# Performance work log

Hardware: AMD Instinct MI355X
Metric: run time of the kernel (lower is better)

## Reference

```python
import jax, jax.numpy as jnp
import numpy as np

EPS = 1e-5  # LayerNorm eps (torch default)
K_NN = 16   # matches init kwarg k


def _knn_idx(pos, k):
    # pos: (B,N,3) -> (B,N,k) indices of k nearest points (sorted by distance,
    # includes self at slot 0), matching pytorch3d knn_points(return_sorted=True).
    sq = jnp.sum(pos * pos, axis=-1)                                   # (B,N)
    d2 = sq[:, :, None] + sq[:, None, :] - 2.0 * jnp.einsum('bnd,bmd->bnm', pos, pos)
    _, idx = jax.lax.top_k(-d2, k)                                     # ascending distance
    return idx


def _gather(feats, idx):
    # feats: (B,N,C), idx: (B,N,K) -> (B,N,K,C)
    return jax.vmap(lambda f, i: f[i])(feats, idx)


def _ln(x, g, b):
    mu = jnp.mean(x, axis=-1, keepdims=True)
    var = jnp.mean((x - mu) ** 2, axis=-1, keepdims=True)
    return (x - mu) * jax.lax.rsqrt(var + EPS) * g + b


def setup_inputs() -> dict:
    key = jax.random.key(0)
    B, N, D, H = 2, 4096, 128, 12
    ks = jax.random.split(key, 16)
    s = 0.05
    f32 = jnp.float32
    return {
        'x': jax.random.normal(ks[0], (B, N, D), f32),
        'pos': jax.random.normal(ks[1], (B, N, 3), f32),
        # linear projections (bias=False)
        'w_q': jax.random.normal(ks[2], (D, D), f32) * s,
        'w_k': jax.random.normal(ks[3], (D, D), f32) * s,
        'w_v': jax.random.normal(ks[4], (D, D), f32) * s,
        # pos_mlp: Linear(3,H) -> LN(H) -> ReLU -> Linear(H,D)
        'pos_w1': jax.random.normal(ks[5], (H, 3), f32) * s,
        'pos_b1': jnp.zeros((H,), f32),
        'pos_g': jnp.ones((H,), f32),
        'pos_beta': jnp.zeros((H,), f32),
        'pos_w2': jax.random.normal(ks[6], (D, H), f32) * s,
        'pos_b2': jnp.zeros((D,), f32),
        # attn_mlp: Linear(D,D) -> LN(D) -> ReLU -> Linear(D,D)
        'attn_w1': jax.random.normal(ks[7], (D, D), f32) * s,
        'attn_b1': jnp.zeros((D,), f32),
        'attn_g': jnp.ones((D,), f32),
        'attn_beta': jnp.zeros((D,), f32),
        'attn_w2': jax.random.normal(ks[8], (D, D), f32) * s,
        'attn_b2': jnp.zeros((D,), f32),
    }


def reference(x, pos, w_q, w_k, w_v,
              pos_w1, pos_b1, pos_g, pos_beta, pos_w2, pos_b2,
              attn_w1, attn_b1, attn_g, attn_beta, attn_w2, attn_b2):
    idx = _knn_idx(pos, K_NN)                        # (B,N,K)
    q = x @ w_q.T                                    # (B,N,D)
    kf = _gather(x @ w_k.T, idx)                     # (B,N,K,D)
    vf = _gather(x @ w_v.T, idx)                     # (B,N,K,D)
    pos_rel = pos[:, :, None, :] - _gather(pos, idx)  # (B,N,K,3)
    # pos_mlp
    pe = _ln(pos_rel @ pos_w1.T + pos_b1, pos_g, pos_beta)
    pe = jax.nn.relu(pe) @ pos_w2.T + pos_b2         # (B,N,K,D)
    # attn_mlp on (q - k + pos_enc)
    w = q[:, :, None, :] - kf + pe
    w = _ln(w @ attn_w1.T + attn_b1, attn_g, attn_beta)
    w = jax.nn.relu(w) @ attn_w2.T + attn_b2         # (B,N,K,D)
    attn = jax.nn.softmax(w, axis=2)                 # softmax over neighbor dim
    return jnp.einsum('bnkd,bnkd->bnd', attn, vf + pe)
```

## Files before the change

### kernel.cpp

```cpp
#include <hip/hip_runtime.h>
#include <hip/hip_bf16.h>
#include <math.h>

#define BATCH 2
#define NPTS 4096
#define DIM 128
#define HID 12
#define KNN 16
#define NSLOT 24
#define BCAP 192
#define BCT 64

#define FOLD_BLOCKS 128
#define M1_BLOCKS 32
#define PRE_BLOCKS (FOLD_BLOCKS + M1_BLOCKS + 4)
#define KNN_BLOCKS (BATCH * NPTS / 4)

typedef __attribute__((ext_vector_type(8))) short short8;
typedef __attribute__((ext_vector_type(4))) float f32x4;

__device__ __forceinline__ short f2b(float f) {
  unsigned u = __float_as_uint(f);
  unsigned r = (u + 0x7fffu + ((u >> 16) & 1u)) >> 16;
  return (short)r;
}
__device__ __forceinline__ float b2f(short h) {
  return __uint_as_float(((unsigned)(unsigned short)h) << 16);
}

#define BITONIC64(v, vi)                                                     \
  {                                                                          \
    _Pragma("unroll") for (int k_ = 2; k_ <= 64; k_ <<= 1) {                 \
      _Pragma("unroll") for (int j_ = k_ >> 1; j_ >= 1; j_ >>= 1) {          \
        const float ov_ = __shfl_xor((v), j_);                               \
        const int oi_ = __shfl_xor((vi), j_);                                \
        const bool up_ = ((lane & k_) == 0);                                 \
        const bool lowpos_ = ((lane & j_) == 0);                             \
        const bool keep_min_ = (lowpos_ == up_);                             \
        const bool lt_ = (ov_ < (v)) || (ov_ == (v) && oi_ < (vi));          \
        const bool take_ = keep_min_ ? lt_ : !lt_;                           \
        if (take_) { (v) = ov_; (vi) = oi_; }                                \
      }                                                                      \
    }                                                                        \
  }

__device__ void knn_body(int bid, const float* __restrict__ pos,
                         int* __restrict__ knn_out) {
  __shared__ float bd_s[4][BCAP];
  __shared__ int bi_s[4][BCAP];

  const int t = threadIdx.x;
  const int w = t >> 6;
  const int lane = t & 63;
  const int n = (bid << 2) + w;
  const int b = n >> 12;
  const int qn = n & (NPTS - 1);

  float* bdl = &bd_s[w][0];
  int* bil = &bi_s[w][0];

  const float* pb = pos + b * NPTS * 3;
  const float qx = pb[qn * 3 + 0];
  const float qy = pb[qn * 3 + 1];
  const float qz = pb[qn * 3 + 2];

  const bool is_slot = (lane < NSLOT);
  float vald, thr;
  int validx;
  int bcount = 0;

  {
    const float2* pp = (const float2*)(pb + lane * 6);
    const float2 u0 = pp[0], u1 = pp[1], u2 = pp[2];
    float dx = qx - u0.x, dy = qy - u0.y, dz = qz - u1.x;
    float v = fmaf(dx, dx, fmaf(dy, dy, dz * dz));
    int vi = lane * 2;
    dx = qx - u1.y; dy = qy - u2.x; dz = qz - u2.y;
    const float d2b = fmaf(dx, dx, fmaf(dy, dy, dz * dz));

    BITONIC64(v, vi)
    vald = is_slot ? v : __builtin_inff();
    validx = is_slot ? vi : 0x7fffffff;
    const float v15 = __shfl(v, 15);
    thr = v15 + v15 * 1e-5f;

    const unsigned long long m = __ballot(d2b < thr);
    if (m) {
      const unsigned lt = __builtin_amdgcn_mbcnt_hi(
          (unsigned)(m >> 32), __builtin_amdgcn_mbcnt_lo((unsigned)m, 0u));
      if (d2b < thr) { bdl[lt] = d2b; bil[lt] = 2 * lane + 1; }
      bcount = (int)__builtin_popcountll(m);
    }
  }

  const float2* pp = (const float2*)(pb + 384 + lane * 6);
  float2 A0 = pp[0], A1 = pp[1], A2 = pp[2];
  pp = (const float2*)(pb + 768 + lane * 6);
  float2 B0 = pp[0], B1 = pp[1], B2 = pp[2];

#pragma unroll 1
  for (int it = 1; it < NPTS / 128; ++it) {
    const float2 c0 = A0, c1v = A1, c2 = A2;
    A0 = B0; A1 = B1; A2 = B2;
    if (it + 2 < NPTS / 128) {
      pp = (const float2*)(pb + (it + 2) * 384 + lane * 6);
      B0 = pp[0]; B1 = pp[1]; B2 = pp[2];
    }
    float dx = qx - c0.x, dy = qy - c0.y, dz = qz - c1v.x;
    const float e2a = fmaf(dx, dx, fmaf(dy, dy, dz * dz));
    dx = qx - c1v.y; dy = qy - c2.x; dz = qz - c2.y;
    const float e2b = fmaf(dx, dx, fmaf(dy, dy, dz * dz));

    if (bcount >= BCT) {
#pragma unroll 1
      while (bcount > 0) {
        const int take = bcount < 40 ? bcount : 40;
        float mv = __builtin_inff();
        int mi = 0x7fffffff;
        if (lane < NSLOT) { mv = vald; mi = validx; }
        else if (lane - NSLOT < take) {
          mv = bdl[bcount - take + lane - NSLOT];
          mi = bil[bcount - take + lane - NSLOT];
        }
        BITONIC64(mv, mi)
        if (is_slot) { vald = mv; validx = mi; }
        bcount -= take;
      }
      const float v15 = __shfl(vald, 15);
      thr = v15 + v15 * 1e-5f;
    }

    {
      const unsigned long long m = __ballot(e2a < thr);
      if (m) {
        const unsigned lt = __builtin_amdgcn_mbcnt_hi(
            (unsigned)(m >> 32), __builtin_amdgcn_mbcnt_lo((unsigned)m, 0u));
        if (e2a < thr) { bdl[bcount + lt] = e2a; bil[bcount + lt] = it * 128 + 2 * lane; }
        bcount += (int)__builtin_popcountll(m);
      }
    }
    {
      const unsigned long long m = __ballot(e2b < thr);
      if (m) {
        const unsigned lt = __builtin_amdgcn_mbcnt_hi(
            (unsigned)(m >> 32), __builtin_amdgcn_mbcnt_lo((unsigned)m, 0u));
        if (e2b < thr) { bdl[bcount + lt] = e2b; bil[bcount + lt] = it * 128 + 2 * lane + 1; }
        bcount += (int)__builtin_popcountll(m);
      }
    }
  }

#pragma unroll 1
  while (bcount > 0) {
    const int take = bcount < 40 ? bcount : 40;
    float mv = __builtin_inff();
    int mi = 0x7fffffff;
    if (lane < NSLOT) { mv = vald; mi = validx; }
    else if (lane - NSLOT < take) {
      mv = bdl[bcount - take + lane - NSLOT];
      mi = bil[bcount - take + lane - NSLOT];
    }
    BITONIC64(mv, mi)
    if (is_slot) { vald = mv; validx = mi; }
    bcount -= take;
  }

  double d2e = 1e300;
  if (is_slot) {
    const double ex = (double)qx - (double)pb[validx * 3 + 0];
    const double ey = (double)qy - (double)pb[validx * 3 + 1];
    const double ez = (double)qz - (double)pb[validx * 3 + 2];
    d2e = ex * ex + ey * ey + ez * ez;
  }
  int rank = 0;
#pragma unroll 1
  for (int j = 0; j < NSLOT; ++j) {
    const double dj = __shfl(d2e, j);
    const int ij = __shfl(validx, j);
    if (dj < d2e || (dj == d2e && ij < validx)) ++rank;
  }
  if (is_slot && rank < KNN) knn_out[((b << 12) + qn) * KNN + rank] = validx;
}

__device__ void fold_body(int bid, const float* __restrict__ aw1,
                          const float* __restrict__ wq, const float* __restrict__ wk,
                          short* __restrict__ WqaHi, short* __restrict__ WqaLo,
                          short* __restrict__ WkaHi, short* __restrict__ WkaLo) {
  const float* w = (bid < 64) ? wq : wk;
  short* oh = (bid < 64) ? WqaHi : WkaHi;
  short* ol = (bid < 64) ? WqaLo : WkaLo;
  const int row = ((bid & 63) << 1) + (threadIdx.x >> 7);
  const int i = threadIdx.x & 127;
  float acc = 0.f;
  for (int j = 0; j < 128; ++j) acc = fmaf(aw1[row * 128 + j], w[j * 128 + i], acc);
  const short h = f2b(acc);
  oh[row * 128 + i] = h;
  ol[row * 128 + i] = f2b(acc - b2f(h));
}

__device__ void m1_body(int bid, const float* __restrict__ aw1,
                        const float* __restrict__ pw2, const float* __restrict__ pb2,
                        const float* __restrict__ ab1,
                        short* __restrict__ M1b, float* __restrict__ c1) {
  const int t = threadIdx.x;
  const int wid = t >> 6, lane = t & 63;
  const int o = bid * 4 + wid;
  const float a0 = aw1[o * 128 + lane];
  const float a1 = aw1[o * 128 + 64 + lane];

  float s = fmaf(a0, pb2[lane], a1 * pb2[64 + lane]);
#pragma unroll
  for (int off = 1; off < 64; off <<= 1) s += __shfl_xor(s, off);
  if (lane == 0) c1[o] = ab1[o] + s;

#pragma unroll
  for (int k = 0; k < HID; ++k) {
    float p = fmaf(a0, pw2[lane * HID + k], a1 * pw2[(64 + lane) * HID + k]);
#pragma unroll
    for (int off = 1; off < 64; off <<= 1) p += __shfl_xor(p, off);
    if (lane == 0) M1b[o * 32 + k] = f2b(p);
  }
  if (lane >= HID && lane < 32) M1b[o * 32 + lane] = 0;
}

__device__ void pw2b_body(const float* __restrict__ pw2, short* __restrict__ pw2b) {
  const int t = threadIdx.x;
  for (int i = t; i < 128 * 32; i += 256) {
    const int o = i >> 5, k = i & 31;
    pw2b[i] = (k < HID) ? f2b(pw2[o * HID + k]) : (short)0;
  }
}
__device__ void aw2b_body(int half, const float* __restrict__ aw2,
                          short* __restrict__ aw2b) {
  const int base = half * 8192;
  for (int i = threadIdx.x; i < 8192; i += 256) aw2b[base + i] = f2b(aw2[base + i]);
}
__device__ void wv_body(const float* __restrict__ wv, short* __restrict__ WvHi,
                        short* __restrict__ WvLo) {
  for (int i = threadIdx.x; i < 128 * 128; i += 256) {
    const float v = wv[i];
    const short h = f2b(v);
    WvHi[i] = h;
    WvLo[i] = f2b(v - b2f(h));
  }
}

__global__ __launch_bounds__(256) void knn_prep_kernel(
    const float* __restrict__ pos, int* __restrict__ knn_out,
    const float* __restrict__ aw1, const float* __restrict__ wq,
    const float* __restrict__ wk,
    short* __restrict__ WqaHi, short* __restrict__ WqaLo,
    short* __restrict__ WkaHi, short* __restrict__ WkaLo,
    const float* __restrict__ pw2, const float* __restrict__ pb2,
    const float* __restrict__ ab1, const float* __restrict__ aw2,
    const float* __restrict__ wv,
    short* __restrict__ M1b, short* __restrict__ pw2b, short* __restrict__ aw2b,
    float* __restrict__ c1, short* __restrict__ WvHi, short* __restrict__ WvLo) {
  const int bid = blockIdx.x;
  if (bid < FOLD_BLOCKS) {
    fold_body(bid, aw1, wq, wk, WqaHi, WqaLo, WkaHi, WkaLo);
  } else if (bid < FOLD_BLOCKS + M1_BLOCKS) {
    m1_body(bid - FOLD_BLOCKS, aw1, pw2, pb2, ab1, M1b, c1);
  } else if (bid == FOLD_BLOCKS + M1_BLOCKS) {
    pw2b_body(pw2, pw2b);
  } else if (bid <= FOLD_BLOCKS + M1_BLOCKS + 2) {
    aw2b_body(bid - (FOLD_BLOCKS + M1_BLOCKS + 1), aw2, aw2b);
  } else if (bid == FOLD_BLOCKS + M1_BLOCKS + 3) {
    wv_body(wv, WvHi, WvLo);
  } else {
    knn_body(bid - PRE_BLOCKS, pos, knn_out);
  }
}

__global__ __launch_bounds__(256) void proj_mfma_kernel(
    const float* __restrict__ x,
    const short* __restrict__ WqaHi, const short* __restrict__ WqaLo,
    const short* __restrict__ WkaHi, const short* __restrict__ WkaLo,
    const short* __restrict__ WvHi, const short* __restrict__ WvLo,
    short* __restrict__ QAb, short* __restrict__ KAb, short* __restrict__ Vpb) {
  const int t = threadIdx.x;
  const int wid = t >> 6, lane = t & 63;
  const int r16 = lane & 15, g4 = lane >> 4;
  const int rowbase = blockIdx.x * 32 + (wid >> 1) * 16;
  const int ch = wid & 1;

  short8 ahi[4], alo[4];
#pragma unroll
  for (int ks = 0; ks < 4; ++ks) {
    const float* xp = x + (rowbase + r16) * DIM + ks * 32 + g4 * 8;
#pragma unroll
    for (int e = 0; e < 8; ++e) {
      const float v = xp[e];
      const short h = f2b(v);
      ahi[ks][e] = h;
      alo[ks][e] = f2b(v - b2f(h));
    }
  }

  const f32x4 zero4 = {0.f, 0.f, 0.f, 0.f};
  const short* WH[3] = {WqaHi, WkaHi, WvHi};
  const short* WL[3] = {WqaLo, WkaLo, WvLo};
  short* OUT[3] = {QAb, KAb, Vpb};
#pragma unroll
  for (int mi = 0; mi < 3; ++mi) {
    const short* wh = WH[mi];
    const short* wl = WL[mi];
    short* o = OUT[mi];
#pragma unroll
    for (int q = 0; q < 4; ++q) {
      const int col = (ch * 4 + q) * 16 + r16;
      f32x4 a = zero4;
#pragma unroll
      for (int ks = 0; ks < 4; ++ks) {
        const short8 bh = *(const short8*)(wh + col * DIM + ks * 32 + g4 * 8);
        const short8 bl = *(const short8*)(wl + col * DIM + ks * 32 + g4 * 8);
        a = __builtin_amdgcn_mfma_f32_16x16x32_bf16(ahi[ks], bh, a, 0, 0, 0);
        a = __builtin_amdgcn_mfma_f32_16x16x32_bf16(alo[ks], bh, a, 0, 0, 0);
        a = __builtin_amdgcn_mfma_f32_16x16x32_bf16(ahi[ks], bl, a, 0, 0, 0);
      }
#pragma unroll
      for (int reg = 0; reg < 4; ++reg)
        o[(rowbase + g4 * 4 + reg) * DIM + (ch * 4 + q) * 16 + r16] = f2b(a[reg]);
    }
  }
}

__global__ __launch_bounds__(256) void pt_wave_kernel(
    const float* __restrict__ pos, const int* __restrict__ knn_in,
    const short* __restrict__ QAb, const short* __restrict__ KAb,
    const short* __restrict__ Vpb,
    const float* __restrict__ pw1, const float* __restrict__ pb1,
    const float* __restrict__ pg, const float* __restrict__ pbeta,
    const float* __restrict__ pb2,
    const float* __restrict__ ag, const float* __restrict__ abeta,
    const float* __restrict__ ab2, const float* __restrict__ c1,
    const short* __restrict__ M1b, const short* __restrict__ pw2b,
    const short* __restrict__ aw2b,
    float* __restrict__ out) {
  __shared__ __align__(16) short z_s[2048];
  __shared__ float red_s[2][4][16];
  __shared__ short hr_s[16][HID];

  const int t = threadIdx.x;
  const int wid = t >> 6;
  const int lane = t & 63;
  const int r16 = lane & 15;
  const int g4 = lane >> 4;
  const int n = blockIdx.x;
  const int b = n >> 12;

  int myidx = 0;
  if (lane < KNN) myidx = knn_in[n * KNN + lane];
  int jC[4];
#pragma unroll
  for (int reg = 0; reg < 4; ++reg) jC[reg] = __shfl(myidx, g4 * 4 + reg);

  const bool pm = (wid == 0) && (lane < 16);

  float rx = 0.f, ry = 0.f, rz = 0.f;
  if (pm) {
    const int jg = b * NPTS + myidx;
    rx = pos[n * 3 + 0] - pos[jg * 3 + 0];
    ry = pos[n * 3 + 1] - pos[jg * 3 + 1];
    rz = pos[n * 3 + 2] - pos[jg * 3 + 2];
  }

  float qa_[2], kav[2][4], vv[2][4];
#pragma unroll
  for (int q = 0; q < 2; ++q) {
    const int o = (wid * 2 + q) * 16 + r16;
    qa_[q] = b2f(QAb[n * DIM + o]);
#pragma unroll
    for (int reg = 0; reg < 4; ++reg) {
      const int row = b * NPTS + jC[reg];
      kav[q][reg] = b2f(KAb[row * DIM + o]);
      vv[q][reg] = b2f(Vpb[row * DIM + o]);
    }
  }

  if (pm) {
    float hr[HID];
    float mu = 0.f;
#pragma unroll
    for (int hh = 0; hh < HID; ++hh) {
      const float v = pb1[hh] + rx * pw1[hh * 3 + 0] + ry * pw1[hh * 3 + 1] +
                      rz * pw1[hh * 3 + 2];
      hr[hh] = v;
      mu += v;
    }
    mu *= (1.f / HID);
    float var = 0.f;
#pragma unroll
    for (int hh = 0; hh < HID; ++hh) { const float d = hr[hh] - mu; var = fmaf(d, d, var); }
    const float rsn = rsqrtf(var * (1.f / HID) + 1e-5f);
#pragma unroll
    for (int hh = 0; hh < HID; ++hh)
      hr_s[lane][hh] = f2b(fmaxf(fmaf((hr[hh] - mu) * rsn, pg[hh], pbeta[hh]), 0.f));
  }
  __syncthreads();

  short8 a1 = {0, 0, 0, 0, 0, 0, 0, 0};
  if (g4 == 0) {
#pragma unroll
    for (int e = 0; e < 8; ++e) a1[e] = hr_s[r16][e];
  } else if (g4 == 1) {
#pragma unroll
    for (int e = 0; e < 4; ++e) a1[e] = hr_s[r16][8 + e];
  }

  const f32x4 zero4 = {0.f, 0.f, 0.f, 0.f};
  f32x4 accw[2], accp[2];
#pragma unroll
  for (int q = 0; q < 2; ++q) {
    const int boff = ((wid * 2 + q) * 16 + r16) * 32 + g4 * 8;
    const short8 bm = *(const short8*)(M1b + boff);
    const short8 bp = *(const short8*)(pw2b + boff);
    accw[q] = __builtin_amdgcn_mfma_f32_16x16x32_bf16(a1, bm, zero4, 0, 0, 0);
    accp[q] = __builtin_amdgcn_mfma_f32_16x16x32_bf16(a1, bp, zero4, 0, 0, 0);
  }

  float w1v[2][4];
#pragma unroll
  for (int q = 0; q < 2; ++q) {
    const int o = (wid * 2 + q) * 16 + r16;
    const float base = qa_[q] + c1[o];
#pragma unroll
    for (int reg = 0; reg < 4; ++reg)
      w1v[q][reg] = accw[q][reg] + base - kav[q][reg];
  }

  {
    float ps[4], pq2[4];
#pragma unroll
    for (int reg = 0; reg < 4; ++reg) {
      ps[reg] = w1v[0][reg] + w1v[1][reg];
      pq2[reg] = fmaf(w1v[0][reg], w1v[0][reg], w1v[1][reg] * w1v[1][reg]);
    }
#pragma unroll
    for (int reg = 0; reg < 4; ++reg) {
#pragma unroll
      for (int off = 1; off <= 8; off <<= 1) {
        ps[reg] += __shfl_xor(ps[reg], off);
        pq2[reg] += __shfl_xor(pq2[reg], off);
      }
    }
    if (r16 == 0) {
#pragma unroll
      for (int reg = 0; reg < 4; ++reg) {
        red_s[0][wid][g4 * 4 + reg] = ps[reg];
        red_s[1][wid][g4 * 4 + reg] = pq2[reg];
      }
    }
  }
  __syncthreads();
  float mu[4], rs[4];
#pragma unroll
  for (int reg = 0; reg < 4; ++reg) {
    const int rr = g4 * 4 + reg;
    const float s = red_s[0][0][rr] + red_s[0][1][rr] + red_s[0][2][rr] + red_s[0][3][rr];
    const float q2 = red_s[1][0][rr] + red_s[1][1][rr] + red_s[1][2][rr] + red_s[1][3][rr];
    mu[reg] = s * (1.f / 128.f);
    const float var = q2 * (1.f / 128.f) - mu[reg] * mu[reg];
    rs[reg] = rsqrtf(var + 1e-5f);
  }

  {
    char* zb = (char*)z_s;
#pragma unroll
    for (int q = 0; q < 2; ++q) {
      const int o = (wid * 2 + q) * 16 + r16;
      const float gam = ag[o], bet = abeta[o];
#pragma unroll
      for (int reg = 0; reg < 4; ++reg) {
        const int rr = g4 * 4 + reg;
        const float zv = fmaxf(fmaf((w1v[q][reg] - mu[reg]) * rs[reg], gam, bet), 0.f);
        unsigned byte = (unsigned)(rr * 256 + o * 2);
        byte ^= ((unsigned)(rr & 7) << 4) ^ ((unsigned)(rr & 8) << 2);
        *(short*)(zb + byte) = f2b(zv);
      }
    }
  }
  __syncthreads();

  short8 a2[4];
  {
    const char* zb = (const char*)z_s;
#pragma unroll
    for (int ks = 0; ks < 4; ++ks) {
      unsigned byte = (unsigned)(r16 * 256 + ks * 64 + g4 * 16);
      byte ^= ((unsigned)(r16 & 7) << 4) ^ ((unsigned)(r16 & 8) << 2);
      a2[ks] = *(const short8*)(zb + byte);
    }
  }

  f32x4 acc2[2] = {zero4, zero4};
#pragma unroll
  for (int q = 0; q < 2; ++q) {
#pragma unroll
    for (int ks = 0; ks < 4; ++ks) {
      const short8 bw =
          *(const short8*)(aw2b + ((wid * 2 + q) * 16 + r16) * DIM + ks * 32 + g4 * 8);
      acc2[q] = __builtin_amdgcn_mfma_f32_16x16x32_bf16(a2[ks], bw, acc2[q], 0, 0, 0);
    }
  }

  float ew[2][4], inv[2];
#pragma unroll
  for (int q = 0; q < 2; ++q) {
    const float bb = ab2[(wid * 2 + q) * 16 + r16];
#pragma unroll
    for (int reg = 0; reg < 4; ++reg) ew[q][reg] = acc2[q][reg] + bb;
    float m = fmaxf(fmaxf(ew[q][0], ew[q][1]), fmaxf(ew[q][2], ew[q][3]));
    m = fmaxf(m, __shfl_xor(m, 16));
    m = fmaxf(m, __shfl_xor(m, 32));
    float s = 0.f;
#pragma unroll
    for (int reg = 0; reg < 4; ++reg) { ew[q][reg] = __expf(ew[q][reg] - m); s += ew[q][reg]; }
    s += __shfl_xor(s, 16);
    s += __shfl_xor(s, 32);
    inv[q] = 1.f / s;
  }

  float o_acc[2];
#pragma unroll
  for (int q = 0; q < 2; ++q) {
    const int o = (wid * 2 + q) * 16 + r16;
    const float pb = pb2[o];
    float acc = 0.f;
#pragma unroll
    for (int reg = 0; reg < 4; ++reg)
      acc = fmaf(ew[q][reg] * inv[q], vv[q][reg] + accp[q][reg] + pb, acc);
    acc += __shfl_xor(acc, 16);
    acc += __shfl_xor(acc, 32);
    o_acc[q] = acc;
  }
  if (g4 < 2) out[n * DIM + (wid * 2 + g4) * 16 + r16] = o_acc[g4];
}

extern "C" void kernel_launch(void* const* d_in, const int* in_sizes, int n_in,
                              void* d_out, int out_size, void* d_ws, size_t ws_size,
                              hipStream_t stream) {
  const float* x   = (const float*)d_in[0];
  const float* pos = (const float*)d_in[1];
  const float* wq  = (const float*)d_in[2];
  const float* wk  = (const float*)d_in[3];
  const float* wv  = (const float*)d_in[4];
  const float* pw1 = (const float*)d_in[5];
  const float* pb1 = (const float*)d_in[6];
  const float* pg  = (const float*)d_in[7];
  const float* pbt = (const float*)d_in[8];
  const float* pw2 = (const float*)d_in[9];
  const float* pb2 = (const float*)d_in[10];
  const float* aw1 = (const float*)d_in[11];
  const float* ab1 = (const float*)d_in[12];
  const float* ag  = (const float*)d_in[13];
  const float* abt = (const float*)d_in[14];
  const float* aw2 = (const float*)d_in[15];
  const float* ab2 = (const float*)d_in[16];
  float* out = (float*)d_out;

  char* ws = (char*)d_ws;
  int*   knn   = (int*)ws;
  short* WqaHi = (short*)(ws + 512u * 1024u);
  short* WqaLo = (short*)(ws + 544u * 1024u);
  short* WkaHi = (short*)(ws + 576u * 1024u);
  short* WkaLo = (short*)(ws + 608u * 1024u);
  short* M1b   = (short*)(ws + 640u * 1024u);
  short* pw2b  = (short*)(ws + 648u * 1024u);
  short* aw2b  = (short*)(ws + 656u * 1024u);
  float* c1    = (float*)(ws + 688u * 1024u);
  short* WvHi  = (short*)(ws + 704u * 1024u);
  short* WvLo  = (short*)(ws + 736u * 1024u);
  short* QAb   = (short*)(ws + (1u << 20));
  short* KAb   = (short*)(ws + 4u * (1u << 20));
  short* Vpb   = (short*)(ws + 7u * (1u << 20));

  knn_prep_kernel<<<PRE_BLOCKS + KNN_BLOCKS, 256, 0, stream>>>(
      pos, knn, aw1, wq, wk, WqaHi, WqaLo, WkaHi, WkaLo, pw2, pb2, ab1, aw2, wv,
      M1b, pw2b, aw2b, c1, WvHi, WvLo);
  proj_mfma_kernel<<<BATCH * NPTS / 32, 256, 0, stream>>>(
      x, WqaHi, WqaLo, WkaHi, WkaLo, WvHi, WvLo, QAb, KAb, Vpb);
  pt_wave_kernel<<<BATCH * NPTS, 256, 0, stream>>>(
      pos, knn, QAb, KAb, Vpb, pw1, pb1, pg, pbt, pb2, ag, abt, ab2, c1,
      M1b, pw2b, aw2b, out);
}
```

Before: 122.1 us.

## Split KNN scan across two waves per query and batch queries per attention block

The KNN search now gives each query point two wavefronts. Each scans half of the candidate points, and the two sorted 24-slot candidate lists are merged through shared memory with one extra bitonic sort before the exact-distance ranking. This halves the serial scan length per wave and doubles the number of KNN blocks. Separately, the attention kernel now loops over 4 query points per block, which cuts launch and block-scheduling overhead but also reduces the number of blocks. The merge adds a block barrier and an extra sort, and the batching adds a serial dependency between query points.

After: 142.0 us. 1.16x slower.

```diff
diff --git a/kernel.cpp b/kernel.cpp
--- a/kernel.cpp
+++ b/kernel.cpp
@@ -10,11 +10,12 @@
 #define NSLOT 24
 #define BCAP 192
 #define BCT 64
+#define PTQ 4
 
 #define FOLD_BLOCKS 128
 #define M1_BLOCKS 32
 #define PRE_BLOCKS (FOLD_BLOCKS + M1_BLOCKS + 4)
-#define KNN_BLOCKS (BATCH * NPTS / 4)
+#define KNN_BLOCKS (BATCH * NPTS / 2)
 
 typedef __attribute__((ext_vector_type(8))) short short8;
 typedef __attribute__((ext_vector_type(4))) float f32x4;
@@ -44,6 +45,17 @@
     }                                                                        \
   }
 
+#define KNN_EVENTS(d2v, base, odd)                                        \
+  {                                                                       \
+    unsigned long long m_ = __ballot((d2v) < thr);                        \
+    if (m_) {                                                             \
+      const unsigned lt_ = __builtin_amdgcn_mbcnt_hi(                     \
+          (unsigned)(m_ >> 32), __builtin_amdgcn_mbcnt_lo((unsigned)m_, 0u)); \
+      if ((d2v) < thr) { bdl[bcount + lt_] = (d2v); bil[bcount + lt_] = (base) + 2 * lane + (odd); } \
+      bcount += (int)__builtin_popcountll(m_);                            \
+    }                                                                     \
+  }
+
 __device__ void knn_body(int bid, const float* __restrict__ pos,
                          int* __restrict__ knn_out) {
   __shared__ float bd_s[4][BCAP];
@@ -52,9 +64,11 @@
   const int t = threadIdx.x;
   const int w = t >> 6;
   const int lane = t & 63;
-  const int n = (bid << 2) + w;
+  const int n = bid * 2 + (w >> 1);
+  const int half = w & 1;
   const int b = n >> 12;
   const int qn = n & (NPTS - 1);
+  const int base0 = half * (NPTS / 2);
 
   float* bdl = &bd_s[w][0];
   int* bil = &bi_s[w][0];
@@ -70,11 +84,11 @@
   int bcount = 0;
 
   {
-    const float2* pp = (const float2*)(pb + lane * 6);
+    const float2* pp = (const float2*)(pb + base0 * 3 + lane * 6);
     const float2 u0 = pp[0], u1 = pp[1], u2 = pp[2];
     float dx = qx - u0.x, dy = qy - u0.y, dz = qz - u1.x;
     float v = fmaf(dx, dx, fmaf(dy, dy, dz * dz));
-    int vi = lane * 2;
+    int vi = base0 + lane * 2;
     dx = qx - u1.y; dy = qy - u2.x; dz = qz - u2.y;
     const float d2b = fmaf(dx, dx, fmaf(dy, dy, dz * dz));
 
@@ -84,26 +98,20 @@
     const float v15 = __shfl(v, 15);
     thr = v15 + v15 * 1e-5f;
 
-    const unsigned long long m = __ballot(d2b < thr);
-    if (m) {
-      const unsigned lt = __builtin_amdgcn_mbcnt_hi(
-          (unsigned)(m >> 32), __builtin_amdgcn_mbcnt_lo((unsigned)m, 0u));
-      if (d2b < thr) { bdl[lt] = d2b; bil[lt] = 2 * lane + 1; }
-      bcount = (int)__builtin_popcountll(m);
-    }
-  }
-
-  const float2* pp = (const float2*)(pb + 384 + lane * 6);
+    KNN_EVENTS(d2b, base0, 1)
+  }
+
+  const float2* pp = (const float2*)(pb + (base0 + 128) * 3 + lane * 6);
   float2 A0 = pp[0], A1 = pp[1], A2 = pp[2];
-  pp = (const float2*)(pb + 768 + lane * 6);
+  pp = (const float2*)(pb + (base0 + 256) * 3 + lane * 6);
   float2 B0 = pp[0], B1 = pp[1], B2 = pp[2];
 
 #pragma unroll 1
-  for (int it = 1; it < NPTS / 128; ++it) {
+  for (int it = 1; it < NPTS / 256; ++it) {
     const float2 c0 = A0, c1v = A1, c2 = A2;
     A0 = B0; A1 = B1; A2 = B2;
-    if (it + 2 < NPTS / 128) {
-      pp = (const float2*)(pb + (it + 2) * 384 + lane * 6);
+    if (it + 2 < NPTS / 256) {
+      pp = (const float2*)(pb + (base0 + (it + 2) * 128) * 3 + lane * 6);
       B0 = pp[0]; B1 = pp[1]; B2 = pp[2];
     }
     float dx = qx - c0.x, dy = qy - c0.y, dz = qz - c1v.x;
@@ -130,24 +138,8 @@
       thr = v15 + v15 * 1e-5f;
     }
 
-    {
-      const unsigned long long m = __ballot(e2a < thr);
-      if (m) {
-        const unsigned lt = __builtin_amdgcn_mbcnt_hi(
-            (unsigned)(m >> 32), __builtin_amdgcn_mbcnt_lo((unsigned)m, 0u));
-        if (e2a < thr) { bdl[bcount + lt] = e2a; bil[bcount + lt] = it * 128 + 2 * lane; }
-        bcount += (int)__builtin_popcountll(m);
-      }
-    }
-    {
-      const unsigned long long m = __ballot(e2b < thr);
-      if (m) {
-        const unsigned lt = __builtin_amdgcn_mbcnt_hi(
-            (unsigned)(m >> 32), __builtin_amdgcn_mbcnt_lo((unsigned)m, 0u));
-        if (e2b < thr) { bdl[bcount + lt] = e2b; bil[bcount + lt] = it * 128 + 2 * lane + 1; }
-        bcount += (int)__builtin_popcountll(m);
-      }
-    }
+    KNN_EVENTS(e2a, base0 + it * 128, 0)
+    KNN_EVENTS(e2b, base0 + it * 128, 1)
   }
 
 #pragma unroll 1
@@ -165,21 +157,34 @@
     bcount -= take;
   }
 
+  if (half == 1 && lane < NSLOT) { bdl[lane] = vald; bil[lane] = validx; }
+  __syncthreads();
+  if (half == 1) return;
+
+  float mv = __builtin_inff();
+  int mi = 0x7fffffff;
+  if (lane < NSLOT) { mv = vald; mi = validx; }
+  else if (lane < 2 * NSLOT) {
+    mv = bd_s[w + 1][lane - NSLOT];
+    mi = bi_s[w + 1][lane - NSLOT];
+  }
+  BITONIC64(mv, mi)
+
   double d2e = 1e300;
   if (is_slot) {
-    const double ex = (double)qx - (double)pb[validx * 3 + 0];
-    const double ey = (double)qy - (double)pb[validx * 3 + 1];
-    const double ez = (double)qz - (double)pb[validx * 3 + 2];
+    const double ex = (double)qx - (double)pb[mi * 3 + 0];
+    const double ey = (double)qy - (double)pb[mi * 3 + 1];
+    const double ez = (double)qz - (double)pb[mi * 3 + 2];
     d2e = ex * ex + ey * ey + ez * ez;
   }
   int rank = 0;
 #pragma unroll 1
   for (int j = 0; j < NSLOT; ++j) {
     const double dj = __shfl(d2e, j);
-    const int ij = __shfl(validx, j);
-    if (dj < d2e || (dj == d2e && ij < validx)) ++rank;
-  }
-  if (is_slot && rank < KNN) knn_out[((b << 12) + qn) * KNN + rank] = validx;
+    const int ij = __shfl(mi, j);
+    if (dj < d2e || (dj == d2e && ij < mi)) ++rank;
+  }
+  if (is_slot && rank < KNN) knn_out[((b << 12) + qn) * KNN + rank] = mi;
 }
 
 __device__ void fold_body(int bid, const float* __restrict__ aw1,
@@ -346,195 +351,199 @@
   const int lane = t & 63;
   const int r16 = lane & 15;
   const int g4 = lane >> 4;
-  const int n = blockIdx.x;
-  const int b = n >> 12;
-
-  int myidx = 0;
-  if (lane < KNN) myidx = knn_in[n * KNN + lane];
-  int jC[4];
-#pragma unroll
-  for (int reg = 0; reg < 4; ++reg) jC[reg] = __shfl(myidx, g4 * 4 + reg);
-
-  const bool pm = (wid == 0) && (lane < 16);
-
-  float rx = 0.f, ry = 0.f, rz = 0.f;
-  if (pm) {
-    const int jg = b * NPTS + myidx;
-    rx = pos[n * 3 + 0] - pos[jg * 3 + 0];
-    ry = pos[n * 3 + 1] - pos[jg * 3 + 1];
-    rz = pos[n * 3 + 2] - pos[jg * 3 + 2];
-  }
-
-  float qa_[2], kav[2][4], vv[2][4];
-#pragma unroll
-  for (int q = 0; q < 2; ++q) {
-    const int o = (wid * 2 + q) * 16 + r16;
-    qa_[q] = b2f(QAb[n * DIM + o]);
-#pragma unroll
-    for (int reg = 0; reg < 4; ++reg) {
-      const int row = b * NPTS + jC[reg];
-      kav[q][reg] = b2f(KAb[row * DIM + o]);
-      vv[q][reg] = b2f(Vpb[row * DIM + o]);
-    }
-  }
-
-  if (pm) {
-    float hr[HID];
-    float mu = 0.f;
-#pragma unroll
-    for (int hh = 0; hh < HID; ++hh) {
-      const float v = pb1[hh] + rx * pw1[hh * 3 + 0] + ry * pw1[hh * 3 + 1] +
-                      rz * pw1[hh * 3 + 2];
-      hr[hh] = v;
-      mu += v;
-    }
-    mu *= (1.f / HID);
-    float var = 0.f;
-#pragma unroll
-    for (int hh = 0; hh < HID; ++hh) { const float d = hr[hh] - mu; var = fmaf(d, d, var); }
-    const float rsn = rsqrtf(var * (1.f / HID) + 1e-5f);
-#pragma unroll
-    for (int hh = 0; hh < HID; ++hh)
-      hr_s[lane][hh] = f2b(fmaxf(fmaf((hr[hh] - mu) * rsn, pg[hh], pbeta[hh]), 0.f));
-  }
-  __syncthreads();
-
-  short8 a1 = {0, 0, 0, 0, 0, 0, 0, 0};
-  if (g4 == 0) {
-#pragma unroll
-    for (int e = 0; e < 8; ++e) a1[e] = hr_s[r16][e];
-  } else if (g4 == 1) {
-#pragma unroll
-    for (int e = 0; e < 4; ++e) a1[e] = hr_s[r16][8 + e];
-  }
-
   const f32x4 zero4 = {0.f, 0.f, 0.f, 0.f};
-  f32x4 accw[2], accp[2];
-#pragma unroll
-  for (int q = 0; q < 2; ++q) {
-    const int boff = ((wid * 2 + q) * 16 + r16) * 32 + g4 * 8;
-    const short8 bm = *(const short8*)(M1b + boff);
-    const short8 bp = *(const short8*)(pw2b + boff);
-    accw[q] = __builtin_amdgcn_mfma_f32_16x16x32_bf16(a1, bm, zero4, 0, 0, 0);
-    accp[q] = __builtin_amdgcn_mfma_f32_16x16x32_bf16(a1, bp, zero4, 0, 0, 0);
-  }
-
-  float w1v[2][4];
-#pragma unroll
-  for (int q = 0; q < 2; ++q) {
-    const int o = (wid * 2 + q) * 16 + r16;
-    const float base = qa_[q] + c1[o];
-#pragma unroll
-    for (int reg = 0; reg < 4; ++reg)
-      w1v[q][reg] = accw[q][reg] + base - kav[q][reg];
-  }
-
-  {
-    float ps[4], pq2[4];
-#pragma unroll
-    for (int reg = 0; reg < 4; ++reg) {
-      ps[reg] = w1v[0][reg] + w1v[1][reg];
-      pq2[reg] = fmaf(w1v[0][reg], w1v[0][reg], w1v[1][reg] * w1v[1][reg]);
-    }
-#pragma unroll
-    for (int reg = 0; reg < 4; ++reg) {
-#pragma unroll
-      for (int off = 1; off <= 8; off <<= 1) {
-        ps[reg] += __shfl_xor(ps[reg], off);
-        pq2[reg] += __shfl_xor(pq2[reg], off);
-      }
-    }
-    if (r16 == 0) {
-#pragma unroll
-      for (int reg = 0; reg < 4; ++reg) {
-        red_s[0][wid][g4 * 4 + reg] = ps[reg];
-        red_s[1][wid][g4 * 4 + reg] = pq2[reg];
-      }
-    }
-  }
-  __syncthreads();
-  float mu[4], rs[4];
-#pragma unroll
-  for (int reg = 0; reg < 4; ++reg) {
-    const int rr = g4 * 4 + reg;
-    const float s = red_s[0][0][rr] + red_s[0][1][rr] + red_s[0][2][rr] + red_s[0][3][rr];
-    const float q2 = red_s[1][0][rr] + red_s[1][1][rr] + red_s[1][2][rr] + red_s[1][3][rr];
-    mu[reg] = s * (1.f / 128.f);
-    const float var = q2 * (1.f / 128.f) - mu[reg] * mu[reg];
-    rs[reg] = rsqrtf(var + 1e-5f);
-  }
-
-  {
-    char* zb = (char*)z_s;
+
+#pragma unroll 1
+  for (int qi = 0; qi < PTQ; ++qi) {
+    const int n = blockIdx.x * PTQ + qi;
+    const int b = n >> 12;
+
+    int myidx = 0;
+    if (lane < KNN) myidx = knn_in[n * KNN + lane];
+    int jC[4];
+#pragma unroll
+    for (int reg = 0; reg < 4; ++reg) jC[reg] = __shfl(myidx, g4 * 4 + reg);
+
+    const bool pm = (wid == 0) && (lane < 16);
+
+    float rx = 0.f, ry = 0.f, rz = 0.f;
+    if (pm) {
+      const int jg = b * NPTS + myidx;
+      rx = pos[n * 3 + 0] - pos[jg * 3 + 0];
+      ry = pos[n * 3 + 1] - pos[jg * 3 + 1];
+      rz = pos[n * 3 + 2] - pos[jg * 3 + 2];
+    }
+
+    float qa_[2], kav[2][4], vv[2][4];
 #pragma unroll
     for (int q = 0; q < 2; ++q) {
       const int o = (wid * 2 + q) * 16 + r16;
-      const float gam = ag[o], bet = abeta[o];
+      qa_[q] = b2f(QAb[n * DIM + o]);
 #pragma unroll
       for (int reg = 0; reg < 4; ++reg) {
-        const int rr = g4 * 4 + reg;
-        const float zv = fmaxf(fmaf((w1v[q][reg] - mu[reg]) * rs[reg], gam, bet), 0.f);
-        unsigned byte = (unsigned)(rr * 256 + o * 2);
-        byte ^= ((unsigned)(rr & 7) << 4) ^ ((unsigned)(rr & 8) << 2);
-        *(short*)(zb + byte) = f2b(zv);
-      }
-    }
-  }
-  __syncthreads();
-
-  short8 a2[4];
-  {
-    const char* zb = (const char*)z_s;
-#pragma unroll
-    for (int ks = 0; ks < 4; ++ks) {
-      unsigned byte = (unsigned)(r16 * 256 + ks * 64 + g4 * 16);
-      byte ^= ((unsigned)(r16 & 7) << 4) ^ ((unsigned)(r16 & 8) << 2);
-      a2[ks] = *(const short8*)(zb + byte);
-    }
-  }
-
-  f32x4 acc2[2] = {zero4, zero4};
-#pragma unroll
-  for (int q = 0; q < 2; ++q) {
-#pragma unroll
-    for (int ks = 0; ks < 4; ++ks) {
-      const short8 bw =
-          *(const short8*)(aw2b + ((wid * 2 + q) * 16 + r16) * DIM + ks * 32 + g4 * 8);
-      acc2[q] = __builtin_amdgcn_mfma_f32_16x16x32_bf16(a2[ks], bw, acc2[q], 0, 0, 0);
-    }
-  }
-
-  float ew[2][4], inv[2];
-#pragma unroll
-  for (int q = 0; q < 2; ++q) {
-    const float bb = ab2[(wid * 2 + q) * 16 + r16];
-#pragma unroll
-    for (int reg = 0; reg < 4; ++reg) ew[q][reg] = acc2[q][reg] + bb;
-    float m = fmaxf(fmaxf(ew[q][0], ew[q][1]), fmaxf(ew[q][2], ew[q][3]));
-    m = fmaxf(m, __shfl_xor(m, 16));
-    m = fmaxf(m, __shfl_xor(m, 32));
-    float s = 0.f;
-#pragma unroll
-    for (int reg = 0; reg < 4; ++reg) { ew[q][reg] = __expf(ew[q][reg] - m); s += ew[q][reg]; }
-    s += __shfl_xor(s, 16);
-    s += __shfl_xor(s, 32);
-    inv[q] = 1.f / s;
-  }
-
-  float o_acc[2];
-#pragma unroll
-  for (int q = 0; q < 2; ++q) {
-    const int o = (wid * 2 + q) * 16 + r16;
-    const float pb = pb2[o];
-    float acc = 0.f;
-#pragma unroll
-    for (int reg = 0; reg < 4; ++reg)
-      acc = fmaf(ew[q][reg] * inv[q], vv[q][reg] + accp[q][reg] + pb, acc);
-    acc += __shfl_xor(acc, 16);
-    acc += __shfl_xor(acc, 32);
-    o_acc[q] = acc;
-  }
-  if (g4 < 2) out[n * DIM + (wid * 2 + g4) * 16 + r16] = o_acc[g4];
+        const int row = b * NPTS + jC[reg];
+        kav[q][reg] = b2f(KAb[row * DIM + o]);
+        vv[q][reg] = b2f(Vpb[row * DIM + o]);
+      }
+    }
+
+    if (pm) {
+      float hr[HID];
+      float mu = 0.f;
+#pragma unroll
+      for (int hh = 0; hh < HID; ++hh) {
+        const float v = pb1[hh] + rx * pw1[hh * 3 + 0] + ry * pw1[hh * 3 + 1] +
+                        rz * pw1[hh * 3 + 2];
+        hr[hh] = v;
+        mu += v;
+      }
+      mu *= (1.f / HID);
+      float var = 0.f;
+#pragma unroll
+      for (int hh = 0; hh < HID; ++hh) { const float d = hr[hh] - mu; var = fmaf(d, d, var); }
+      const float rsn = rsqrtf(var * (1.f / HID) + 1e-5f);
+#pragma unroll
+      for (int hh = 0; hh < HID; ++hh)
+        hr_s[lane][hh] = f2b(fmaxf(fmaf((hr[hh] - mu) * rsn, pg[hh], pbeta[hh]), 0.f));
+    }
+    __syncthreads();
+
+    short8 a1 = {0, 0, 0, 0, 0, 0, 0, 0};
+    if (g4 == 0) {
+#pragma unroll
+      for (int e = 0; e < 8; ++e) a1[e] = hr_s[r16][e];
+    } else if (g4 == 1) {
+#pragma unroll
+      for (int e = 0; e < 4; ++e) a1[e] = hr_s[r16][8 + e];
+    }
+
+    f32x4 accw[2], accp[2];
+#pragma unroll
+    for (int q = 0; q < 2; ++q) {
+      const int boff = ((wid * 2 + q) * 16 + r16) * 32 + g4 * 8;
+      const short8 bm = *(const short8*)(M1b + boff);
+      const short8 bp = *(const short8*)(pw2b + boff);
+      accw[q] = __builtin_amdgcn_mfma_f32_16x16x32_bf16(a1, bm, zero4, 0, 0, 0);
+      accp[q] = __builtin_amdgcn_mfma_f32_16x16x32_bf16(a1, bp, zero4, 0, 0, 0);
+    }
+
+    float w1v[2][4];
+#pragma unroll
+    for (int q = 0; q < 2; ++q) {
+      const int o = (wid * 2 + q) * 16 + r16;
+      const float base = qa_[q] + c1[o];
+#pragma unroll
+      for (int reg = 0; reg < 4; ++reg)
+        w1v[q][reg] = accw[q][reg] + base - kav[q][reg];
+    }
+
+    {
+      float ps[4], pq2[4];
+#pragma unroll
+      for (int reg = 0; reg < 4; ++reg) {
+        ps[reg] = w1v[0][reg] + w1v[1][reg];
+        pq2[reg] = fmaf(w1v[0][reg], w1v[0][reg], w1v[1][reg] * w1v[1][reg]);
+      }
+#pragma unroll
+      for (int reg = 0; reg < 4; ++reg) {
+#pragma unroll
+        for (int off = 1; off <= 8; off <<= 1) {
+          ps[reg] += __shfl_xor(ps[reg], off);
+          pq2[reg] += __shfl_xor(pq2[reg], off);
+        }
+      }
+      if (r16 == 0) {
+#pragma unroll
+        for (int reg = 0; reg < 4; ++reg) {
+          red_s[0][wid][g4 * 4 + reg] = ps[reg];
+          red_s[1][wid][g4 * 4 + reg] = pq2[reg];
+        }
+      }
+    }
+    __syncthreads();
+    float mu[4], rs[4];
+#pragma unroll
+    for (int reg = 0; reg < 4; ++reg) {
+      const int rr = g4 * 4 + reg;
+      const float s = red_s[0][0][rr] + red_s[0][1][rr] + red_s[0][2][rr] + red_s[0][3][rr];
+      const float q2 = red_s[1][0][rr] + red_s[1][1][rr] + red_s[1][2][rr] + red_s[1][3][rr];
+      mu[reg] = s * (1.f / 128.f);
+      const float var = q2 * (1.f / 128.f) - mu[reg] * mu[reg];
+      rs[reg] = rsqrtf(var + 1e-5f);
+    }
+
+    {
+      char* zb = (char*)z_s;
+#pragma unroll
+      for (int q = 0; q < 2; ++q) {
+        const int o = (wid * 2 + q) * 16 + r16;
+        const float gam = ag[o], bet = abeta[o];
+#pragma unroll
+        for (int reg = 0; reg < 4; ++reg) {
+          const int rr = g4 * 4 + reg;
+          const float zv = fmaxf(fmaf((w1v[q][reg] - mu[reg]) * rs[reg], gam, bet), 0.f);
+          unsigned byte = (unsigned)(rr * 256 + o * 2);
+          byte ^= ((unsigned)(rr & 7) << 4) ^ ((unsigned)(rr & 8) << 2);
+          *(short*)(zb + byte) = f2b(zv);
+        }
+      }
+    }
+    __syncthreads();
+
+    short8 a2[4];
+    {
+      const char* zb = (const char*)z_s;
+#pragma unroll
+      for (int ks = 0; ks < 4; ++ks) {
+        unsigned byte = (unsigned)(r16 * 256 + ks * 64 + g4 * 16);
+        byte ^= ((unsigned)(r16 & 7) << 4) ^ ((unsigned)(r16 & 8) << 2);
+        a2[ks] = *(const short8*)(zb + byte);
+      }
+    }
+
+    f32x4 acc2[2] = {zero4, zero4};
+#pragma unroll
+    for (int q = 0; q < 2; ++q) {
+#pragma unroll
+      for (int ks = 0; ks < 4; ++ks) {
+        const short8 bw =
+            *(const short8*)(aw2b + ((wid * 2 + q) * 16 + r16) * DIM + ks * 32 + g4 * 8);
+        acc2[q] = __builtin_amdgcn_mfma_f32_16x16x32_bf16(a2[ks], bw, acc2[q], 0, 0, 0);
+      }
+    }
+
+    float ew[2][4], inv[2];
+#pragma unroll
+    for (int q = 0; q < 2; ++q) {
+      const float bb = ab2[(wid * 2 + q) * 16 + r16];
+#pragma unroll
+      for (int reg = 0; reg < 4; ++reg) ew[q][reg] = acc2[q][reg] + bb;
+      float m = fmaxf(fmaxf(ew[q][0], ew[q][1]), fmaxf(ew[q][2], ew[q][3]));
+      m = fmaxf(m, __shfl_xor(m, 16));
+      m = fmaxf(m, __shfl_xor(m, 32));
+      float s = 0.f;
+#pragma unroll
+      for (int reg = 0; reg < 4; ++reg) { ew[q][reg] = __expf(ew[q][reg] - m); s += ew[q][reg]; }
+      s += __shfl_xor(s, 16);
+      s += __shfl_xor(s, 32);
+      inv[q] = 1.f / s;
+    }
+
+    float o_acc[2];
+#pragma unroll
+    for (int q = 0; q < 2; ++q) {
+      const int o = (wid * 2 + q) * 16 + r16;
+      const float pb = pb2[o];
+      float acc = 0.f;
+#pragma unroll
+      for (int reg = 0; reg < 4; ++reg)
+        acc = fmaf(ew[q][reg] * inv[q], vv[q][reg] + accp[q][reg] + pb, acc);
+      acc += __shfl_xor(acc, 16);
+      acc += __shfl_xor(acc, 32);
+      o_acc[q] = acc;
+    }
+    if (g4 < 2) out[n * DIM + (wid * 2 + g4) * 16 + r16] = o_acc[g4];
+  }
 }
 
 extern "C" void kernel_launch(void* const* d_in, const int* in_sizes, int n_in,
@@ -580,7 +589,7 @@
       M1b, pw2b, aw2b, c1, WvHi, WvLo);
   proj_mfma_kernel<<<BATCH * NPTS / 32, 256, 0, stream>>>(
       x, WqaHi, WqaLo, WkaHi, WkaLo, WvHi, WvLo, QAb, KAb, Vpb);
-  pt_wave_kernel<<<BATCH * NPTS, 256, 0, stream>>>(
+  pt_wave_kernel<<<BATCH * NPTS / PTQ, 256, 0, stream>>>(
       pos, knn, QAb, KAb, Vpb, pw1, pb1, pg, pbt, pb2, ag, abt, ab2, c1,
       M1b, pw2b, aw2b, out);
 }
```
